# Kernel tuning notes

Measured on AMD Instinct MI355X. Metric: run time of the kernel, lower is better.

Reference implementation:

```python
import jax, jax.numpy as jnp
import numpy as np

HEADS = 16
HEAD_DIM = 64
EMB = 1024
B, S = 4, 2048
SCALE = 1.0 / 8.0  # fixed constant in the original code
MASK_PENALTY = -50.0  # original adds -50 * upper_triangular, not -inf


def setup_inputs() -> dict:
    key = jax.random.key(0)
    ks = jax.random.split(key, 5)
    x = jax.random.normal(ks[0], (B, S, EMB), dtype=jnp.float32)
    Wq = jax.random.normal(ks[1], (EMB, HEADS * HEAD_DIM), dtype=jnp.float32) * 0.02
    Wk = jax.random.normal(ks[2], (EMB, HEADS * HEAD_DIM), dtype=jnp.float32) * 0.02
    Wv = jax.random.normal(ks[3], (EMB, HEADS * HEAD_DIM), dtype=jnp.float32) * 0.02
    Wr = jax.random.normal(ks[4], (HEADS * HEAD_DIM, EMB), dtype=jnp.float32) * 0.02
    return {"x": x, "Wq": Wq, "Wk": Wk, "Wv": Wv, "Wr": Wr}


def reference(x, Wq, Wk, Wv, Wr):
    b, s, _ = x.shape
    # project and split heads: [b, s, h, d]
    q = (x @ Wq).reshape(b, s, HEADS, HEAD_DIM)
    k = (x @ Wk).reshape(b, s, HEADS, HEAD_DIM)
    v = (x @ Wv).reshape(b, s, HEADS, HEAD_DIM)
    # scores: [b, h, s, s]
    scores = SCALE * jnp.einsum('bqhd,bkhd->bhqk', q, k)
    # causal additive mask: -50 on strictly-upper triangle (faithful to original)
    causal = jnp.triu(jnp.ones((s, s), dtype=x.dtype), k=1)
    scores = scores + MASK_PENALTY * causal
    attn = jax.nn.softmax(scores, axis=-1)
    out = jnp.einsum('bhqk,bkhd->bqhd', attn, v).reshape(b, s, HEADS * HEAD_DIM)
    return out @ Wr
```

## Files before the change

kernel.cpp:

```cpp
#include <hip/hip_runtime.h>

typedef _Float16 f16;
typedef _Float16 f16x8 __attribute__((ext_vector_type(8)));
typedef _Float16 f16x4 __attribute__((ext_vector_type(4)));
typedef float f32x4 __attribute__((ext_vector_type(4)));
typedef float f32x16 __attribute__((ext_vector_type(16)));

#define MFMA16(A, B, C) __builtin_amdgcn_mfma_f32_16x16x32_f16((A), (B), (C), 0, 0, 0)
#define MFMA32(A, B, C) __builtin_amdgcn_mfma_f32_32x32x16_f16((A), (B), (C), 0, 0, 0)
#define MFMA16K16(A, B, C) __builtin_amdgcn_mfma_f32_16x16x16f16((A), (B), (C), 0, 0, 0)

__device__ __forceinline__ void async16(void* lds, const void* gp) {
    __builtin_amdgcn_global_load_lds(
        (__attribute__((address_space(1))) void*)(gp),
        (__attribute__((address_space(3))) void*)(lds), 16, 0, 0);
}

__global__ __launch_bounds__(256) void k_convert(const float* __restrict__ in,
                                                 f16* __restrict__ out, int n) {
    int i = (blockIdx.x * 256 + threadIdx.x) * 4;
    if (i + 3 < n) {
        float4 v = *(const float4*)(in + i);
        f16x4 o = {(f16)v.x, (f16)v.y, (f16)v.z, (f16)v.w};
        *(f16x4*)(out + i) = o;
    }
}

__global__ __launch_bounds__(256) void k_transpose_w4(const float* __restrict__ Wq,
                                                      const float* __restrict__ Wk,
                                                      const float* __restrict__ Wv,
                                                      const float* __restrict__ Wr,
                                                      f16* __restrict__ Wqkvt,
                                                      f16* __restrict__ Wrt) {
    __shared__ float tile[32][33];
    int z = blockIdx.z;
    const float* W = (z == 0) ? Wq : (z == 1) ? Wk : (z == 2) ? Wv : Wr;
    f16* Wt = (z == 3) ? Wrt : Wqkvt + z * 1048576;
    int c0 = blockIdx.x * 32, r0 = blockIdx.y * 32;
    int tx = threadIdx.x, ty = threadIdx.y;
#pragma unroll
    for (int j = 0; j < 32; j += 8)
        tile[ty + j][tx] = W[(r0 + ty + j) * 1024 + c0 + tx];
    __syncthreads();
#pragma unroll
    for (int j = 0; j < 32; j += 8)
        Wt[(c0 + ty + j) * 1024 + r0 + tx] = (f16)tile[tx][ty + j];
}

__global__ __launch_bounds__(256) void k_transpose_v(const f16* __restrict__ QKV,
                                                     f16* __restrict__ Vt) {
    __shared__ f16 tile[32][33];
    int s0 = blockIdx.x * 32;
    int d0 = blockIdx.y * 32;
    int bh = blockIdx.z;
    int b = bh >> 4, h = bh & 15;
    int tx = threadIdx.x, ty = threadIdx.y;
#pragma unroll
    for (int j = 0; j < 32; j += 8)
        tile[ty + j][tx] = QKV[(b * 2048 + s0 + ty + j) * 3072 + 2048 + h * 64 + d0 + tx];
    __syncthreads();
#pragma unroll
    for (int j = 0; j < 32; j += 8)
        Vt[(bh * 64 + d0 + ty + j) * 2048 + s0 + tx] = tile[tx][ty + j];
}

template <bool OUT_F16>
__global__ __launch_bounds__(256, 4) void k_gemm_bt(const f16* __restrict__ A,
                                                    const f16* __restrict__ Bt,
                                                    void* __restrict__ Cv,
                                                    int M, int N, int K) {
    __shared__ f16 As[128][32];
    __shared__ f16 Bs[128][32];
    int t = threadIdx.x;
    int lane = t & 63, w = t >> 6;
    int wm = (w >> 1) * 64, wn = (w & 1) * 64;
    int m0 = blockIdx.y * 128, n0 = blockIdx.x * 128;
    int ln = lane & 31, kh = lane >> 5;
    int sw = (ln >> 1) & 3;

    int lin0 = w * 128 + lane, lin1 = lin0 + 64;
    int r0 = lin0 >> 2, c0 = (lin0 & 3) ^ ((r0 >> 1) & 3);
    int r1 = lin1 >> 2, c1 = (lin1 & 3) ^ ((r1 >> 1) & 3);
    const f16* gA0 = A + (size_t)(m0 + r0) * K + c0 * 8;
    const f16* gA1 = A + (size_t)(m0 + r1) * K + c1 * 8;
    const f16* gB0 = Bt + (size_t)(n0 + r0) * K + c0 * 8;
    const f16* gB1 = Bt + (size_t)(n0 + r1) * K + c1 * 8;
    f16* lA0 = &As[0][0] + w * 1024;
    f16* lB0 = &Bs[0][0] + w * 1024;

    f32x16 acc[2][2] = {};

    for (int k0 = 0; k0 < K; k0 += 32) {
        __syncthreads();
        async16(lA0, gA0 + k0);
        async16(lA0 + 512, gA1 + k0);
        async16(lB0, gB0 + k0);
        async16(lB0 + 512, gB1 + k0);
        __syncthreads();
#pragma unroll
        for (int kd = 0; kd < 2; kd++) {
            int c = kd * 2 + kh;
            f16x8 af[2], bf[2];
#pragma unroll
            for (int mt = 0; mt < 2; mt++)
                af[mt] = *(const f16x8*)&As[wm + mt * 32 + ln][(c ^ sw) * 8];
#pragma unroll
            for (int nt = 0; nt < 2; nt++)
                bf[nt] = *(const f16x8*)&Bs[wn + nt * 32 + ln][(c ^ sw) * 8];
#pragma unroll
            for (int mt = 0; mt < 2; mt++)
#pragma unroll
                for (int nt = 0; nt < 2; nt++)
                    acc[mt][nt] = MFMA32(af[mt], bf[nt], acc[mt][nt]);
        }
    }

#pragma unroll
    for (int mt = 0; mt < 2; mt++)
#pragma unroll
        for (int nt = 0; nt < 2; nt++)
#pragma unroll
            for (int r = 0; r < 16; r++) {
                int row = m0 + wm + mt * 32 + (r & 3) + 8 * (r >> 2) + 4 * kh;
                int col = n0 + wn + nt * 32 + ln;
                float v = acc[mt][nt][r];
                if (OUT_F16)
                    ((f16*)Cv)[(size_t)row * N + col] = (f16)v;
                else
                    ((float*)Cv)[(size_t)row * N + col] = v;
            }
}

__global__ __launch_bounds__(256, 2) void k_attn(const f16* __restrict__ QKV,
                                                 const f16* __restrict__ Vt,
                                                 float* __restrict__ Oacc,
                                                 float* __restrict__ Lacc) {
    __shared__ f16 Ks[64][72];
    __shared__ f16 Vs[64][72];
    int bh = blockIdx.x;
    int p = blockIdx.y & 3, khalf = blockIdx.y >> 2;
    int b = bh >> 4, h = bh & 15;
    int t = threadIdx.x, lane = t & 63, wq = t >> 6;
    int ln = lane & 15, g = lane >> 4, g8 = g * 8, rg = g * 4;

    int kr0 = t >> 3, kc0 = (t & 7) * 8;
    int kr1 = (t + 256) >> 3, kc1 = (t & 7) * 8;
    const f16* Kbase = QKV + (size_t)b * 2048 * 3072 + 1024 + h * 64;
    const f16* Vbase = Vt + (size_t)bh * 64 * 2048;

    const float C_SCL = 0.18033688f;
    const float C_MSK = -72.134752f;
    f16x4 ones4 = {(f16)1.f, (f16)1.f, (f16)1.f, (f16)1.f};

    int qtA = 7 - p, nkA = 4 * qtA + 4, cntA = nkA >> 1, sA = khalf * cntA;
    int qtB = p,     nkB = 4 * qtB + 4, cntB = nkB >> 1, sB = khalf * cntB;

    int4 rk0, rk1, rv0, rv1;
    {
        int kk = sA * 64;
        rk0 = *(const int4*)(Kbase + (size_t)(kk + kr0) * 3072 + kc0);
        rk1 = *(const int4*)(Kbase + (size_t)(kk + kr1) * 3072 + kc1);
        rv0 = *(const int4*)(Vbase + (size_t)kr0 * 2048 + kk + kc0);
        rv1 = *(const int4*)(Vbase + (size_t)kr1 * 2048 + kk + kc1);
    }

    for (int phase = 0; phase < 2; phase++) {
        int qt = phase ? qtB : qtA;
        int s = phase ? sB : sA;
        int cnt = phase ? cntB : cntA;
        int q0 = qt * 256;
        int qw = q0 + wq * 64;

        f16x8 bq[4][2];
#pragma unroll
        for (int nt = 0; nt < 4; nt++)
#pragma unroll
            for (int kd = 0; kd < 2; kd++)
                bq[nt][kd] = *(const f16x8*)(QKV +
                    (size_t)(b * 2048 + qw + nt * 16 + ln) * 3072 + h * 64 + kd * 32 + g8);

        f32x4 oacc[4][4] = {};
        f32x4 osum[4] = {};

        for (int j = 0; j < cnt; j++) {
            int k0 = (s + j) * 64;
            __syncthreads();
            *(int4*)&Ks[kr0][kc0] = rk0;
            *(int4*)&Ks[kr1][kc1] = rk1;
            *(int4*)&Vs[kr0][kc0] = rv0;
            *(int4*)&Vs[kr1][kc1] = rv1;
            int nxt = (j + 1 < cnt) ? (s + j + 1) : ((phase == 0) ? sB : -1);
            if (nxt >= 0) {
                int kk = nxt * 64;
                rk0 = *(const int4*)(Kbase + (size_t)(kk + kr0) * 3072 + kc0);
                rk1 = *(const int4*)(Kbase + (size_t)(kk + kr1) * 3072 + kc1);
                rv0 = *(const int4*)(Vbase + (size_t)kr0 * 2048 + kk + kc0);
                rv1 = *(const int4*)(Vbase + (size_t)kr1 * 2048 + kk + kc1);
            }
            __syncthreads();

            if (k0 > qw + 63) continue;

            f32x4 sacc[4][4] = {};
#pragma unroll
            for (int kd = 0; kd < 2; kd++) {
                f16x8 ak[4];
#pragma unroll
                for (int mt = 0; mt < 4; mt++)
                    ak[mt] = *(const f16x8*)&Ks[mt * 16 + ln][kd * 32 + g8];
#pragma unroll
                for (int mt = 0; mt < 4; mt++)
#pragma unroll
                    for (int nt = 0; nt < 4; nt++)
                        sacc[mt][nt] = MFMA16(ak[mt], bq[nt][kd], sacc[mt][nt]);
            }

            bool needs_mask = (k0 + 63 > qw);
            f16x4 pk[4][4];
#pragma unroll
            for (int nt = 0; nt < 4; nt++) {
                int q = qw + nt * 16 + ln;
#pragma unroll
                for (int mt = 0; mt < 4; mt++) {
#pragma unroll
                    for (int r = 0; r < 4; r++) {
                        float e;
                        if (needs_mask) {
                            int kk = k0 + mt * 16 + rg + r;
                            e = __builtin_amdgcn_exp2f(
                                fmaf(sacc[mt][nt][r], C_SCL, (kk > q) ? C_MSK : 0.f));
                        } else {
                            e = __builtin_amdgcn_exp2f(sacc[mt][nt][r] * C_SCL);
                        }
                        pk[mt][nt][r] = (f16)e;
                    }
                }
            }

#pragma unroll
            for (int mt = 0; mt < 4; mt++) {
                f16x4 bv[4];
#pragma unroll
                for (int dt = 0; dt < 4; dt++)
                    bv[dt] = *(const f16x4*)&Vs[dt * 16 + ln][mt * 16 + rg];
#pragma unroll
                for (int nt = 0; nt < 4; nt++) {
#pragma unroll
                    for (int dt = 0; dt < 4; dt++)
                        oacc[nt][dt] = MFMA16K16(pk[mt][nt], bv[dt], oacc[nt][dt]);
                    osum[nt] = MFMA16K16(pk[mt][nt], ones4, osum[nt]);
                }
            }
        }

#pragma unroll
        for (int nt = 0; nt < 4; nt++)
#pragma unroll
            for (int r = 0; r < 4; r++) {
                int q = qw + nt * 16 + rg + r;
                size_t row = (size_t)(b * 2048 + q);
#pragma unroll
                for (int dt = 0; dt < 4; dt++)
                    atomicAdd(&Oacc[row * 1024 + h * 64 + dt * 16 + ln],
                              oacc[nt][dt][r]);
                if (ln == 0)
                    atomicAdd(&Lacc[(size_t)bh * 2048 + q], osum[nt][r]);
            }
    }
}

__global__ __launch_bounds__(256) void k_finalize(const float* __restrict__ Oacc,
                                                  const float* __restrict__ Lacc,
                                                  f16* __restrict__ Ob) {
    int i = (blockIdx.x * 256 + threadIdx.x) * 4;
    int row = i >> 10, col = i & 1023;
    int b = row >> 11, q = row & 2047, h = col >> 6;
    float inv = __builtin_amdgcn_rcpf(Lacc[(size_t)(b * 16 + h) * 2048 + q]);
    float4 v = *(const float4*)(Oacc + i);
    f16x4 o = {(f16)(v.x * inv), (f16)(v.y * inv), (f16)(v.z * inv), (f16)(v.w * inv)};
    *(f16x4*)(Ob + i) = o;
}

extern "C" void kernel_launch(void* const* d_in, const int* in_sizes, int n_in,
                              void* d_out, int out_size, void* d_ws, size_t ws_size,
                              hipStream_t stream) {
    const float* x = (const float*)d_in[0];
    const float* Wq = (const float*)d_in[1];
    const float* Wk = (const float*)d_in[2];
    const float* Wv = (const float*)d_in[3];
    const float* Wr = (const float*)d_in[4];
    float* out = (float*)d_out;

    f16* ws = (f16*)d_ws;
    f16* xb    = ws;
    f16* Wqkvt = xb + 8388608;
    f16* Wrt   = Wqkvt + 3145728;
    f16* QKVb  = Wrt + 1048576;
    f16* Vtb   = QKVb + 25165824;
    f16* Obuf  = Vtb + 8388608;
    float* Lacc = (float*)(Obuf + 8388608);
    float* Oacc = out;

    k_convert<<<8192, 256, 0, stream>>>(x, xb, 8388608);
    dim3 tb(32, 8);
    k_transpose_w4<<<dim3(32, 32, 4), tb, 0, stream>>>(Wq, Wk, Wv, Wr, Wqkvt, Wrt);
    k_gemm_bt<true><<<dim3(24, 64), 256, 0, stream>>>(xb, Wqkvt, QKVb, 8192, 3072, 1024);
    k_transpose_v<<<dim3(64, 2, 64), tb, 0, stream>>>(QKVb, Vtb);
    hipMemsetAsync(Oacc, 0, (size_t)8388608 * 4, stream);
    hipMemsetAsync(Lacc, 0, (size_t)131072 * 4, stream);
    k_attn<<<dim3(64, 8), 256, 0, stream>>>(QKVb, Vtb, Oacc, Lacc);
    k_finalize<<<8192, 256, 0, stream>>>(Oacc, Lacc, Obuf);
    k_gemm_bt<false><<<dim3(8, 64), 256, 0, stream>>>(Obuf, Wrt, out, 8192, 1024, 1024);
}
```

Baseline: 321.9 us.

## Restructure attention into single-wave blocks reading K/V directly from global memory

The attention kernel moves from 256-thread blocks sharing K/V tiles in LDS to 64-thread single-wave blocks. Each wave handles 32 query rows and loads K and V fragments straight from global memory, with no barriers. Per-wave causal bounds skip fully masked key tiles. The row sum moves from an extra MFMA against a ones vector to scalar accumulation plus a shuffle reduction. This removes the LDS staging and synchronisation and raises the block count, but loses K/V reuse across waves, so global and cache traffic rise.

Measured after the change: 412.4 us. 28.1% more time.

```diff
diff --git a/kernel.cpp b/kernel.cpp
--- a/kernel.cpp
+++ b/kernel.cpp
@@ -131,97 +131,86 @@
             }
 }
 
-__global__ __launch_bounds__(256, 2) void k_attn(const f16* __restrict__ QKV,
-                                                 const f16* __restrict__ Vt,
-                                                 float* __restrict__ Oacc,
-                                                 float* __restrict__ Lacc) {
-    __shared__ f16 Ks[64][72];
-    __shared__ f16 Vs[64][72];
+__global__ __launch_bounds__(64) void k_attn(const f16* __restrict__ QKV,
+                                             const f16* __restrict__ Vt,
+                                             float* __restrict__ Oacc,
+                                             float* __restrict__ Lacc) {
     int bh = blockIdx.x;
-    int p = blockIdx.y & 3, khalf = blockIdx.y >> 2;
+    int y = blockIdx.y;
+    int khalf = y >> 5;
+    int p = (y >> 2) & 7;
+    int wq = y & 3;
     int b = bh >> 4, h = bh & 15;
-    int t = threadIdx.x, lane = t & 63, wq = t >> 6;
+    int lane = threadIdx.x;
     int ln = lane & 15, g = lane >> 4, g8 = g * 8, rg = g * 4;
 
-    int kr0 = t >> 3, kc0 = (t & 7) * 8;
-    int kr1 = (t + 256) >> 3, kc1 = (t & 7) * 8;
     const f16* Kbase = QKV + (size_t)b * 2048 * 3072 + 1024 + h * 64;
     const f16* Vbase = Vt + (size_t)bh * 64 * 2048;
 
     const float C_SCL = 0.18033688f;
     const float C_MSK = -72.134752f;
-    f16x4 ones4 = {(f16)1.f, (f16)1.f, (f16)1.f, (f16)1.f};
-
-    int qtA = 7 - p, nkA = 4 * qtA + 4, cntA = nkA >> 1, sA = khalf * cntA;
-    int qtB = p,     nkB = 4 * qtB + 4, cntB = nkB >> 1, sB = khalf * cntB;
-
-    int4 rk0, rk1, rv0, rv1;
-    {
-        int kk = sA * 64;
-        rk0 = *(const int4*)(Kbase + (size_t)(kk + kr0) * 3072 + kc0);
-        rk1 = *(const int4*)(Kbase + (size_t)(kk + kr1) * 3072 + kc1);
-        rv0 = *(const int4*)(Vbase + (size_t)kr0 * 2048 + kk + kc0);
-        rv1 = *(const int4*)(Vbase + (size_t)kr1 * 2048 + kk + kc1);
-    }
+
+    int vko[4], vvo[4];
+#pragma unroll
+    for (int mt = 0; mt < 4; mt++) vko[mt] = (mt * 16 + ln) * 3072 + g8;
+#pragma unroll
+    for (int dt = 0; dt < 4; dt++) vvo[dt] = (dt * 16 + ln) * 2048 + rg;
 
     for (int phase = 0; phase < 2; phase++) {
-        int qt = phase ? qtB : qtA;
-        int s = phase ? sB : sA;
-        int cnt = phase ? cntB : cntA;
-        int q0 = qt * 256;
-        int qw = q0 + wq * 64;
-
-        f16x8 bq[4][2];
-#pragma unroll
-        for (int nt = 0; nt < 4; nt++)
+        int qt = phase ? p : (15 - p);
+        int q0 = qt * 128;
+        int qw = q0 + wq * 32;
+        int cnt = qt + 1;
+        int s = khalf * cnt;
+        int jhi = 2 * qt + (wq >> 1);
+        int cntw = jhi - s + 1;
+        cntw = cntw < 0 ? 0 : (cntw > cnt ? cnt : cntw);
+
+        f16x8 bq[2][2];
+#pragma unroll
+        for (int nt = 0; nt < 2; nt++)
 #pragma unroll
             for (int kd = 0; kd < 2; kd++)
                 bq[nt][kd] = *(const f16x8*)(QKV +
                     (size_t)(b * 2048 + qw + nt * 16 + ln) * 3072 + h * 64 + kd * 32 + g8);
 
-        f32x4 oacc[4][4] = {};
-        f32x4 osum[4] = {};
-
-        for (int j = 0; j < cnt; j++) {
+        f32x4 oacc[2][4] = {};
+        float lsum[2] = {0.f, 0.f};
+
+        for (int j = 0; j < cntw; j++) {
             int k0 = (s + j) * 64;
-            __syncthreads();
-            *(int4*)&Ks[kr0][kc0] = rk0;
-            *(int4*)&Ks[kr1][kc1] = rk1;
-            *(int4*)&Vs[kr0][kc0] = rv0;
-            *(int4*)&Vs[kr1][kc1] = rv1;
-            int nxt = (j + 1 < cnt) ? (s + j + 1) : ((phase == 0) ? sB : -1);
-            if (nxt >= 0) {
-                int kk = nxt * 64;
-                rk0 = *(const int4*)(Kbase + (size_t)(kk + kr0) * 3072 + kc0);
-                rk1 = *(const int4*)(Kbase + (size_t)(kk + kr1) * 3072 + kc1);
-                rv0 = *(const int4*)(Vbase + (size_t)kr0 * 2048 + kk + kc0);
-                rv1 = *(const int4*)(Vbase + (size_t)kr1 * 2048 + kk + kc1);
-            }
-            __syncthreads();
-
-            if (k0 > qw + 63) continue;
-
-            f32x4 sacc[4][4] = {};
-#pragma unroll
-            for (int kd = 0; kd < 2; kd++) {
-                f16x8 ak[4];
+            const f16* Kp = Kbase + (size_t)k0 * 3072;
+            const f16* Vp = Vbase + k0;
+
+            f16x8 ak[2][4];
+#pragma unroll
+            for (int mt = 0; mt < 4; mt++)
+#pragma unroll
+                for (int kd = 0; kd < 2; kd++)
+                    ak[kd][mt] = *(const f16x8*)(Kp + vko[mt] + kd * 32);
+            f16x4 bv[4][4];
+#pragma unroll
+            for (int mt = 0; mt < 4; mt++)
+#pragma unroll
+                for (int dt = 0; dt < 4; dt++)
+                    bv[mt][dt] = *(const f16x4*)(Vp + vvo[dt] + mt * 16);
+
+            f32x4 sacc[4][2] = {};
+#pragma unroll
+            for (int kd = 0; kd < 2; kd++)
 #pragma unroll
                 for (int mt = 0; mt < 4; mt++)
-                    ak[mt] = *(const f16x8*)&Ks[mt * 16 + ln][kd * 32 + g8];
-#pragma unroll
-                for (int mt = 0; mt < 4; mt++)
-#pragma unroll
-                    for (int nt = 0; nt < 4; nt++)
-                        sacc[mt][nt] = MFMA16(ak[mt], bq[nt][kd], sacc[mt][nt]);
-            }
+#pragma unroll
+                    for (int nt = 0; nt < 2; nt++)
+                        sacc[mt][nt] = MFMA16(ak[kd][mt], bq[nt][kd], sacc[mt][nt]);
 
             bool needs_mask = (k0 + 63 > qw);
-            f16x4 pk[4][4];
-#pragma unroll
-            for (int nt = 0; nt < 4; nt++) {
-                int q = qw + nt * 16 + ln;
-#pragma unroll
-                for (int mt = 0; mt < 4; mt++) {
+#pragma unroll
+            for (int mt = 0; mt < 4; mt++) {
+                f16x4 pk[2];
+#pragma unroll
+                for (int nt = 0; nt < 2; nt++) {
+                    int q = qw + nt * 16 + ln;
 #pragma unroll
                     for (int r = 0; r < 4; r++) {
                         float e;
@@ -232,29 +221,28 @@
                         } else {
                             e = __builtin_amdgcn_exp2f(sacc[mt][nt][r] * C_SCL);
                         }
-                        pk[mt][nt][r] = (f16)e;
+                        lsum[nt] += e;
+                        pk[nt][r] = (f16)e;
                     }
                 }
-            }
-
-#pragma unroll
-            for (int mt = 0; mt < 4; mt++) {
-                f16x4 bv[4];
-#pragma unroll
-                for (int dt = 0; dt < 4; dt++)
-                    bv[dt] = *(const f16x4*)&Vs[dt * 16 + ln][mt * 16 + rg];
-#pragma unroll
-                for (int nt = 0; nt < 4; nt++) {
+#pragma unroll
+                for (int nt = 0; nt < 2; nt++)
 #pragma unroll
                     for (int dt = 0; dt < 4; dt++)
-                        oacc[nt][dt] = MFMA16K16(pk[mt][nt], bv[dt], oacc[nt][dt]);
-                    osum[nt] = MFMA16K16(pk[mt][nt], ones4, osum[nt]);
-                }
+                        oacc[nt][dt] = MFMA16K16(pk[nt], bv[mt][dt], oacc[nt][dt]);
             }
         }
 
 #pragma unroll
-        for (int nt = 0; nt < 4; nt++)
+        for (int nt = 0; nt < 2; nt++) {
+            float rs = lsum[nt];
+            rs += __shfl_xor(rs, 16, 64);
+            rs += __shfl_xor(rs, 32, 64);
+            lsum[nt] = rs;
+        }
+
+#pragma unroll
+        for (int nt = 0; nt < 2; nt++)
 #pragma unroll
             for (int r = 0; r < 4; r++) {
                 int q = qw + nt * 16 + rg + r;
@@ -263,9 +251,12 @@
                 for (int dt = 0; dt < 4; dt++)
                     atomicAdd(&Oacc[row * 1024 + h * 64 + dt * 16 + ln],
                               oacc[nt][dt][r]);
-                if (ln == 0)
-                    atomicAdd(&Lacc[(size_t)bh * 2048 + q], osum[nt][r]);
             }
+        if (g == 0) {
+#pragma unroll
+            for (int nt = 0; nt < 2; nt++)
+                atomicAdd(&Lacc[(size_t)bh * 2048 + qw + nt * 16 + ln], lsum[nt]);
+        }
     }
 }
 
@@ -308,7 +299,7 @@
     k_transpose_v<<<dim3(64, 2, 64), tb, 0, stream>>>(QKVb, Vtb);
     hipMemsetAsync(Oacc, 0, (size_t)8388608 * 4, stream);
     hipMemsetAsync(Lacc, 0, (size_t)131072 * 4, stream);
-    k_attn<<<dim3(64, 8), 256, 0, stream>>>(QKVb, Vtb, Oacc, Lacc);
+    k_attn<<<dim3(64, 64), 64, 0, stream>>>(QKVb, Vtb, Oacc, Lacc);
     k_finalize<<<8192, 256, 0, stream>>>(Oacc, Lacc, Obuf);
     k_gemm_bt<false><<<dim3(8, 64), 256, 0, stream>>>(Obuf, Wrt, out, 8192, 1024, 1024);
 }
```
